# Optimization experiments

Hardware: AMD Instinct MI355X
Metric: run time of the kernel (lower is better)

Reference implementation:

```python
import jax, jax.numpy as jnp
import numpy as np
import math

NUM_HEADS = 16
MAX_BIAS = 8.0

def _alibi_slopes(n_heads):
    def slopes(n):
        start = 2.0 ** (-2 ** (-(math.log2(n) - 3)))
        return [start * start ** i for i in range(n)]
    if math.log2(n_heads).is_integer():
        s = slopes(n_heads)
    else:
        p = 2 ** math.floor(math.log2(n_heads))
        s = slopes(p) + slopes(2 * p)[0::2][: n_heads - p]
    return jnp.asarray(np.array(s, dtype=np.float32))

def setup_inputs() -> dict:
    key = jax.random.key(0)
    ks = jax.random.split(key, 5)
    B, S, C = 2, 2048, 1024
    return {
        "x": jax.random.normal(ks[0], (B, S, C), jnp.float32),
        "in_proj_weight": jax.random.normal(ks[1], (3 * C, C), jnp.float32) * (C ** -0.5),
        "in_proj_bias": jax.random.normal(ks[2], (3 * C,), jnp.float32) * 0.02,
        "out_proj_weight": jax.random.normal(ks[3], (C, C), jnp.float32) * (C ** -0.5),
        "out_proj_bias": jax.random.normal(ks[4], (C,), jnp.float32) * 0.02,
    }

def reference(x, in_proj_weight, in_proj_bias, out_proj_weight, out_proj_bias):
    B, S, C = x.shape
    H = NUM_HEADS
    D = C // H
    # fused qkv projection: [B,S,3C] -> [3,B,H,S,D]
    qkv = x @ in_proj_weight.T + in_proj_bias
    qkv = qkv.reshape(B, S, 3, H, D).transpose(2, 0, 3, 1, 4)
    q, k, v = qkv[0], qkv[1], qkv[2]
    # ALiBi bias: slopes[h] * (i - j), clamped above at MAX_BIAS -> [H,S,S]
    slopes = _alibi_slopes(H)
    pos = jnp.arange(S, dtype=jnp.float32)
    rel = pos[:, None] - pos[None, :]  # [S,S]
    bias = jnp.minimum(rel[None, :, :] * slopes[:, None, None], MAX_BIAS)
    # scores [B,H,S,S]
    scores = jnp.einsum("bhqd,bhkd->bhqk", q, k) * (D ** -0.5) + bias[None]
    probs = jax.nn.softmax(scores, axis=-1)
    out = jnp.einsum("bhqk,bhkd->bhqd", probs, v)
    out = out.transpose(0, 2, 1, 3).reshape(B, S, C)
    return out @ out_proj_weight.T + out_proj_bias
```

## Files before the change

### kernel.cpp

```cpp
#include <hip/hip_runtime.h>
#include <hip/hip_bf16.h>

typedef __bf16 bf16;
typedef __bf16 bf16x8 __attribute__((ext_vector_type(8)));
typedef __bf16 bf16x4 __attribute__((ext_vector_type(4)));
typedef float  f32x4  __attribute__((ext_vector_type(4)));

#define LOG2E 1.44269504088896340736f


__device__ __forceinline__ void gl_lds16(const void* g, void* l) {
  __builtin_amdgcn_global_load_lds((__attribute__((address_space(1))) void*)g,
                                   (__attribute__((address_space(3))) void*)l,
                                   16, 0, 0);
}

__global__ void cvt3_kernel(const float* __restrict__ x,
                            const float* __restrict__ w1,
                            const float* __restrict__ w2,
                            bf16* __restrict__ xb,
                            bf16* __restrict__ w1b,
                            bf16* __restrict__ w2b) {
  const int NX = 1048576, NW1 = 786432, NW2 = 262144;
  const int total = NX + NW1 + NW2;
  int i = blockIdx.x * blockDim.x + threadIdx.x;
  const int stride = gridDim.x * blockDim.x;
  for (; i < total; i += stride) {
    const float* s; bf16* d; int j;
    if (i < NX)            { s = x;  d = xb;  j = i; }
    else if (i < NX + NW1) { s = w1; d = w1b; j = i - NX; }
    else                   { s = w2; d = w2b; j = i - NX - NW1; }
    f32x4 v = ((const f32x4*)s)[j];
    bf16x4 o;
    o[0] = (bf16)v[0]; o[1] = (bf16)v[1]; o[2] = (bf16)v[2]; o[3] = (bf16)v[3];
    ((bf16x4*)d)[j] = o;
  }
}

template<int EPI>
__global__ __launch_bounds__(256) void gemm_bt(const bf16* __restrict__ A,
                                               const bf16* __restrict__ Bw,
                                               const float* __restrict__ bias,
                                               void* __restrict__ outp,
                                               int M, int N, int K) {
  __shared__ bf16 As[128 * 64];
  __shared__ bf16 Bs[128 * 64];
  const int tid  = threadIdx.x;
  const int lane = tid & 63;
  const int w    = tid >> 6;
  const int wm   = w >> 1, wn = w & 1;
  const int mBase = blockIdx.y * 128;
  const int nBase = blockIdx.x * 128;
  const int rl = lane & 15;
  const int qg = lane >> 4;
  const int srow = tid >> 3;
  const int schunk = tid & 7;

  f32x4 acc[4][4] = {};

  for (int k0 = 0; k0 < K; k0 += 64) {
    __syncthreads();
#pragma unroll
    for (int rr = 0; rr < 4; ++rr) {
      int r  = rr * 32 + srow;
      int cs = schunk ^ (r & 7);
      gl_lds16(A  + (size_t)(mBase + r) * K + k0 + cs * 8, As + r * 64 + schunk * 8);
      gl_lds16(Bw + (size_t)(nBase + r) * K + k0 + cs * 8, Bs + r * 64 + schunk * 8);
    }
    __syncthreads();
#pragma unroll
    for (int ks = 0; ks < 2; ++ks) {
      bf16x8 af[4], bfr[4];
      const int cl = ks * 4 + qg;
#pragma unroll
      for (int mf = 0; mf < 4; ++mf) {
        int r = wm * 64 + mf * 16 + rl;
        af[mf] = *(const bf16x8*)(As + r * 64 + (cl ^ (r & 7)) * 8);
      }
#pragma unroll
      for (int nf = 0; nf < 4; ++nf) {
        int r = wn * 64 + nf * 16 + rl;
        bfr[nf] = *(const bf16x8*)(Bs + r * 64 + (cl ^ (r & 7)) * 8);
      }
#pragma unroll
      for (int mf = 0; mf < 4; ++mf)
#pragma unroll
        for (int nf = 0; nf < 4; ++nf)
          acc[mf][nf] = __builtin_amdgcn_mfma_f32_16x16x32_bf16(af[mf], bfr[nf],
                                                                acc[mf][nf], 0, 0, 0);
    }
  }

#pragma unroll
  for (int mf = 0; mf < 4; ++mf) {
#pragma unroll
    for (int nf = 0; nf < 4; ++nf) {
      int n = nBase + wn * 64 + nf * 16 + rl;
      float bv = bias[n];
#pragma unroll
      for (int j = 0; j < 4; ++j) {
        int m = mBase + wm * 64 + mf * 16 + qg * 4 + j;
        float val = acc[mf][nf][j] + bv;
        if (EPI == 0) {
          int t = n >> 10, rem = n & 1023;
          int h = rem >> 6, d = rem & 63;
          int b = m >> 11, s = m & 2047;
          bf16* q = (bf16*)outp;
          size_t hb = (size_t)(b * 16 + h);
          if (t == 0) {
            q[(hb * 2048 + s) * 64 + d] = (bf16)(val * (0.125f * LOG2E));
          } else if (t == 1) {
            q[4194304 + (hb * 2048 + s) * 64 + d] = (bf16)val;
          } else {
            q[8388608 + (hb * 64 + d) * 2048 + s] = (bf16)val;
          }
        } else {
          ((float*)outp)[(size_t)m * N + n] = val;
        }
      }
    }
  }
}

__global__ __launch_bounds__(256) void attn_kernel(const bf16* __restrict__ qkv,
                                                   bf16* __restrict__ attout) {
  constexpr int S = 2048;
  __shared__ bf16 Ks[64 * 64];
  __shared__ bf16 Vt[80 * 64];
  __shared__ bf16 Ps[4][16 * 72];

  const int tid  = threadIdx.x;
  const int lane = tid & 63;
  const int w    = tid >> 6;
  const int qt   = blockIdx.x;
  const int bh   = blockIdx.y;
  const int h    = bh & 15;
  const size_t headoff = (size_t)bh * 131072;
  const bf16* Qg = qkv + headoff;
  const bf16* Kg = qkv + 4194304 + headoff;
  const bf16* Vg = qkv + 8388608 + headoff;

  const int rl = lane & 15;
  const int qg = lane >> 4;
  const int srow = tid >> 3;
  const int schunk = tid & 7;

  for (int i = tid; i < 16 * 64; i += 256)
    Vt[64 * 64 + i] = (i < 64) ? (bf16)1.0f : (bf16)0.0f;

  bf16x8 qf[2];
  {
    int row = qt * 64 + w * 16 + rl;
    qf[0] = *(const bf16x8*)(Qg + (size_t)row * 64 + qg * 8);
    qf[1] = *(const bf16x8*)(Qg + (size_t)row * 64 + 32 + qg * 8);
  }

  const float slope2 = exp2f(-0.5f * (float)(h + 1)) * LOG2E;
  const float MB2 = 8.0f * LOG2E;
  float arow[4], bcol[4];
#pragma unroll
  for (int j = 0; j < 4; ++j)
    arow[j] = slope2 * (float)(qt * 64 + w * 16 + qg * 4 + j);
#pragma unroll
  for (int cf = 0; cf < 4; ++cf)
    bcol[cf] = slope2 * (float)(cf * 16 + rl);
  const float kstep = slope2 * 64.0f;

  f32x4 o[5] = {};
  float m2[4];
#pragma unroll
  for (int j = 0; j < 4; ++j) m2[j] = -__builtin_inff();

  for (int kb = 0; kb < S; kb += 64) {
    __syncthreads();
#pragma unroll
    for (int rr = 0; rr < 2; ++rr) {
      int r  = rr * 32 + srow;
      int cs = schunk ^ (r & 7);
      gl_lds16(Kg + (size_t)(kb + r) * 64 + cs * 8, Ks + r * 64 + schunk * 8);
      gl_lds16(Vg + (size_t)r * 2048 + kb + cs * 8, Vt + r * 64 + schunk * 8);
    }
    __syncthreads();

    f32x4 sc[4] = {};
#pragma unroll
    for (int cf = 0; cf < 4; ++cf) {
      int r = cf * 16 + rl;
#pragma unroll
      for (int ks = 0; ks < 2; ++ks) {
        int cl = ks * 4 + qg;
        bf16x8 kf = *(const bf16x8*)(Ks + r * 64 + (cl ^ (r & 7)) * 8);
        sc[cf] = __builtin_amdgcn_mfma_f32_16x16x32_bf16(qf[ks], kf, sc[cf], 0, 0, 0);
      }
    }

    float pv[4][4], mx[4];
#pragma unroll
    for (int j = 0; j < 4; ++j) mx[j] = -__builtin_inff();
#pragma unroll
    for (int cf = 0; cf < 4; ++cf)
#pragma unroll
      for (int j = 0; j < 4; ++j) {
        float t = sc[cf][j] + fminf(arow[j] - bcol[cf], MB2);
        pv[cf][j] = t;
        mx[j] = fmaxf(mx[j], t);
      }
#pragma unroll
    for (int off = 1; off < 16; off <<= 1)
#pragma unroll
      for (int j = 0; j < 4; ++j)
        mx[j] = fmaxf(mx[j], __shfl_xor(mx[j], off, 16));

    float g = fmaxf(fmaxf(mx[0] - m2[0], mx[1] - m2[1]),
                    fmaxf(mx[2] - m2[2], mx[3] - m2[3]));
    g = fmaxf(g, __shfl_xor(g, 16));
    g = fmaxf(g, __shfl_xor(g, 32));
    if (g > 8.0f) {
#pragma unroll
      for (int j = 0; j < 4; ++j) {
        float mn = fmaxf(m2[j], mx[j]);
        float alpha = exp2f(m2[j] - mn);
        m2[j] = mn;
#pragma unroll
        for (int dg = 0; dg < 5; ++dg)
          o[dg][j] *= alpha;
      }
    }

#pragma unroll
    for (int cf = 0; cf < 4; ++cf)
#pragma unroll
      for (int j = 0; j < 4; ++j) {
        float p = exp2f(pv[cf][j] - m2[j]);
        Ps[w][(qg * 4 + j) * 72 + cf * 16 + rl] = (bf16)p;
      }

    __builtin_amdgcn_wave_barrier();

#pragma unroll
    for (int kc = 0; kc < 2; ++kc) {
      bf16x8 pa = *(const bf16x8*)(&Ps[w][rl * 72 + kc * 32 + qg * 8]);
#pragma unroll
      for (int dg = 0; dg < 5; ++dg) {
        int row = dg * 16 + rl;
        bf16x8 vb = *(const bf16x8*)(Vt + row * 64 + ((kc * 4 + qg) ^ (row & 7)) * 8);
        o[dg] = __builtin_amdgcn_mfma_f32_16x16x32_bf16(pa, vb, o[dg], 0, 0, 0);
      }
    }

#pragma unroll
    for (int cf = 0; cf < 4; ++cf) bcol[cf] += kstep;
  }

  float inv[4];
#pragma unroll
  for (int j = 0; j < 4; ++j)
    inv[j] = 1.0f / __shfl(o[4][j], lane & 48);

  const int b = bh >> 4;
#pragma unroll
  for (int dg = 0; dg < 4; ++dg)
#pragma unroll
    for (int j = 0; j < 4; ++j) {
      int row = qt * 64 + w * 16 + qg * 4 + j;
      int col = h * 64 + dg * 16 + rl;
      attout[((size_t)b * 2048 + row) * 1024 + col] = (bf16)(o[dg][j] * inv[j]);
    }
}

extern "C" void kernel_launch(void* const* d_in, const int* in_sizes, int n_in,
                              void* d_out, int out_size, void* d_ws, size_t ws_size,
                              hipStream_t stream) {
  const float* x  = (const float*)d_in[0];
  const float* w1 = (const float*)d_in[1];
  const float* b1 = (const float*)d_in[2];
  const float* w2 = (const float*)d_in[3];
  const float* b2 = (const float*)d_in[4];
  float* out = (float*)d_out;

  char* ws = (char*)d_ws;
  bf16* xb    = (bf16*)(ws);
  bf16* w1b   = (bf16*)(ws + 8388608);
  bf16* w2b   = (bf16*)(ws + 14680064);
  bf16* qkvb  = (bf16*)(ws + 16777216);
  bf16* attnb = (bf16*)(ws + 41943040);

  cvt3_kernel<<<2048, 256, 0, stream>>>(x, w1, w2, xb, w1b, w2b);
  gemm_bt<0><<<dim3(24, 32), 256, 0, stream>>>(xb, w1b, b1, (void*)qkvb, 4096, 3072, 1024);
  attn_kernel<<<dim3(32, 32), 256, 0, stream>>>(qkvb, attnb);
  gemm_bt<1><<<dim3(8, 32), 256, 0, stream>>>(attnb, w2b, b2, (void*)out, 4096, 1024, 1024);
}
```

Measured before the change: 171.0 us.

## Keep softmax probabilities in registers via transposed QK^T and 16x16x16 MFMA for PV

Swaps the QK^T MFMA operands so each lane holds scores in the layout needed as the A operand of a 16x16x16 bf16 MFMA. The probabilities then feed PV straight from registers, which removes the per-wave LDS staging buffer and its wave barrier. The online softmax is reduced to a single wave-wide max with a shared rescale, and the bias term is folded into a running base offset. The change also precomputes LDS offsets, remaps blocks so heads interleave, and fills the extra V rows with ones for the row sum. In exchange it uses twice as many smaller MFMAs for PV and a coarser shared max, which carries some numerical risk.

```diff
diff --git a/kernel.cpp b/kernel.cpp
--- a/kernel.cpp
+++ b/kernel.cpp
@@ -5,6 +5,7 @@
 typedef __bf16 bf16x8 __attribute__((ext_vector_type(8)));
 typedef __bf16 bf16x4 __attribute__((ext_vector_type(4)));
 typedef float  f32x4  __attribute__((ext_vector_type(4)));
+typedef short  s16x4  __attribute__((ext_vector_type(4)));
 
 #define LOG2E 1.44269504088896340736f
 
@@ -13,6 +14,23 @@
   __builtin_amdgcn_global_load_lds((__attribute__((address_space(1))) void*)g,
                                    (__attribute__((address_space(3))) void*)l,
                                    16, 0, 0);
+}
+
+#if __has_builtin(__builtin_amdgcn_mfma_f32_16x16x16bf16_1k)
+__device__ __forceinline__ f32x4 mfma16(s16x4 a, s16x4 b, f32x4 c) {
+  return __builtin_amdgcn_mfma_f32_16x16x16bf16_1k(a, b, c, 0, 0, 0);
+}
+#else
+__device__ __forceinline__ f32x4 mfma16(s16x4 a, s16x4 b, f32x4 c) {
+  f32x4 d;
+  asm volatile("v_mfma_f32_16x16x16_bf16 %0, %1, %2, %3\n\ts_nop 7\n\ts_nop 3"
+               : "=v"(d) : "v"(a), "v"(b), "v"(c));
+  return d;
+}
+#endif
+
+__device__ __forceinline__ s16x4 as_s16x4(bf16x4 v) {
+  union { bf16x4 h; s16x4 s; } u; u.h = v; return u.s;
 }
 
 __global__ void cvt3_kernel(const float* __restrict__ x,
@@ -127,14 +145,14 @@
   constexpr int S = 2048;
   __shared__ bf16 Ks[64 * 64];
   __shared__ bf16 Vt[80 * 64];
-  __shared__ bf16 Ps[4][16 * 72];
 
   const int tid  = threadIdx.x;
   const int lane = tid & 63;
   const int w    = tid >> 6;
-  const int qt   = blockIdx.x;
-  const int bh   = blockIdx.y;
-  const int h    = bh & 15;
+  const int id = blockIdx.x;
+  const int bh = (id & 7) * 4 + ((id >> 3) & 3);
+  const int qt = id >> 5;
+  const int h  = bh & 15;
   const size_t headoff = (size_t)bh * 131072;
   const bf16* Qg = qkv + headoff;
   const bf16* Kg = qkv + 4194304 + headoff;
@@ -146,116 +164,121 @@
   const int schunk = tid & 7;
 
   for (int i = tid; i < 16 * 64; i += 256)
-    Vt[64 * 64 + i] = (i < 64) ? (bf16)1.0f : (bf16)0.0f;
-
+    Vt[64 * 64 + i] = (bf16)1.0f;
+
+  const int qrow = qt * 64 + w * 16 + rl;
   bf16x8 qf[2];
-  {
-    int row = qt * 64 + w * 16 + rl;
-    qf[0] = *(const bf16x8*)(Qg + (size_t)row * 64 + qg * 8);
-    qf[1] = *(const bf16x8*)(Qg + (size_t)row * 64 + 32 + qg * 8);
-  }
+  qf[0] = *(const bf16x8*)(Qg + (size_t)qrow * 64 + qg * 8);
+  qf[1] = *(const bf16x8*)(Qg + (size_t)qrow * 64 + 32 + qg * 8);
+
+  int koff[4][2];
+#pragma unroll
+  for (int cf = 0; cf < 4; ++cf) {
+    int r = cf * 16 + rl, r7 = r & 7;
+#pragma unroll
+    for (int ks = 0; ks < 2; ++ks)
+      koff[cf][ks] = r * 64 + (((ks * 4 + qg) ^ r7) << 3);
+  }
+  int voff[4][5];
+#pragma unroll
+  for (int dg = 0; dg < 5; ++dg) {
+    int row = dg * 16 + rl, r7 = row & 7;
+#pragma unroll
+    for (int cf = 0; cf < 4; ++cf)
+      voff[cf][dg] = row * 64 + ((((cf << 1) + (qg >> 1)) ^ r7) << 3) + ((qg & 1) << 2);
+  }
+
+  const int cs8 = (schunk ^ (srow & 7)) * 8;
+  const bf16* ksrc = Kg + (size_t)srow * 64 + cs8;
+  const bf16* vsrc = Vg + (size_t)srow * 2048 + cs8;
+  bf16* kdst = Ks + srow * 64 + schunk * 8;
+  bf16* vdst = Vt + srow * 64 + schunk * 8;
 
   const float slope2 = exp2f(-0.5f * (float)(h + 1)) * LOG2E;
-  const float MB2 = 8.0f * LOG2E;
-  float arow[4], bcol[4];
+  const float nslope = -slope2;
+  const float kstep  = slope2 * 64.0f;
+  float basep = slope2 * (float)(qrow - qg * 4);
+  float Mm    = 8.0f * LOG2E;
+
+  f32x4 o[5] = {};
+
+  for (int kt = 0; kt < S / 64; ++kt) {
+    __syncthreads();
+    gl_lds16(ksrc,             kdst);
+    gl_lds16(ksrc + 32 * 64,   kdst + 32 * 64);
+    gl_lds16(vsrc,             vdst);
+    gl_lds16(vsrc + 32 * 2048, vdst + 32 * 64);
+    ksrc += 64 * 64; vsrc += 64;
+    __syncthreads();
+
+    f32x4 sc[4] = {};
+#pragma unroll
+    for (int cf = 0; cf < 4; ++cf)
+#pragma unroll
+      for (int ks = 0; ks < 2; ++ks) {
+        bf16x8 kf = *(const bf16x8*)(Ks + koff[cf][ks]);
+        sc[cf] = __builtin_amdgcn_mfma_f32_16x16x32_bf16(kf, qf[ks], sc[cf], 0, 0, 0);
+      }
+
+    float t[4][4];
+#pragma unroll
+    for (int cf = 0; cf < 4; ++cf)
+#pragma unroll
+      for (int j = 0; j < 4; ++j)
+        t[cf][j] = sc[cf][j] + fminf(__builtin_fmaf(nslope, (float)(cf * 16 + j), basep), Mm);
+
+    float mxa = fmaxf(fmaxf(t[0][0], t[0][1]), fmaxf(t[0][2], t[0][3]));
+    float mxb = fmaxf(fmaxf(t[1][0], t[1][1]), fmaxf(t[1][2], t[1][3]));
+    float mxc = fmaxf(fmaxf(t[2][0], t[2][1]), fmaxf(t[2][2], t[2][3]));
+    float mxd = fmaxf(fmaxf(t[3][0], t[3][1]), fmaxf(t[3][2], t[3][3]));
+    float mx = fmaxf(fmaxf(mxa, mxb), fmaxf(mxc, mxd));
+    mx = fmaxf(mx, __shfl_xor(mx, 16));
+    mx = fmaxf(mx, __shfl_xor(mx, 32));
+
+    bf16x4 pav[4];
+    if (__any(mx > 8.0f)) {
+      float d = fmaxf(mx, 0.0f);
+      basep -= d; Mm -= d;
+      float alpha = exp2f(-d);
+      float av[4];
+#pragma unroll
+      for (int j = 0; j < 4; ++j)
+        av[j] = __shfl(alpha, qg * 4 + j);
+#pragma unroll
+      for (int dg = 0; dg < 5; ++dg)
+#pragma unroll
+        for (int j = 0; j < 4; ++j)
+          o[dg][j] *= av[j];
+#pragma unroll
+      for (int cf = 0; cf < 4; ++cf)
+#pragma unroll
+        for (int j = 0; j < 4; ++j)
+          pav[cf][j] = (bf16)exp2f(t[cf][j] - d);
+    } else {
+#pragma unroll
+      for (int cf = 0; cf < 4; ++cf)
+#pragma unroll
+        for (int j = 0; j < 4; ++j)
+          pav[cf][j] = (bf16)exp2f(t[cf][j]);
+    }
+
+#pragma unroll
+    for (int cf = 0; cf < 4; ++cf) {
+      s16x4 pa = as_s16x4(pav[cf]);
+#pragma unroll
+      for (int dg = 0; dg < 5; ++dg) {
+        s16x4 vb = *(const s16x4*)(Vt + voff[cf][dg]);
+        o[dg] = mfma16(pa, vb, o[dg]);
+      }
+    }
+
+    basep -= kstep;
+  }
+
+  float inv[4];
 #pragma unroll
   for (int j = 0; j < 4; ++j)
-    arow[j] = slope2 * (float)(qt * 64 + w * 16 + qg * 4 + j);
-#pragma unroll
-  for (int cf = 0; cf < 4; ++cf)
-    bcol[cf] = slope2 * (float)(cf * 16 + rl);
-  const float kstep = slope2 * 64.0f;
-
-  f32x4 o[5] = {};
-  float m2[4];
-#pragma unroll
-  for (int j = 0; j < 4; ++j) m2[j] = -__builtin_inff();
-
-  for (int kb = 0; kb < S; kb += 64) {
-    __syncthreads();
-#pragma unroll
-    for (int rr = 0; rr < 2; ++rr) {
-      int r  = rr * 32 + srow;
-      int cs = schunk ^ (r & 7);
-      gl_lds16(Kg + (size_t)(kb + r) * 64 + cs * 8, Ks + r * 64 + schunk * 8);
-      gl_lds16(Vg + (size_t)r * 2048 + kb + cs * 8, Vt + r * 64 + schunk * 8);
-    }
-    __syncthreads();
-
-    f32x4 sc[4] = {};
-#pragma unroll
-    for (int cf = 0; cf < 4; ++cf) {
-      int r = cf * 16 + rl;
-#pragma unroll
-      for (int ks = 0; ks < 2; ++ks) {
-        int cl = ks * 4 + qg;
-        bf16x8 kf = *(const bf16x8*)(Ks + r * 64 + (cl ^ (r & 7)) * 8);
-        sc[cf] = __builtin_amdgcn_mfma_f32_16x16x32_bf16(qf[ks], kf, sc[cf], 0, 0, 0);
-      }
-    }
-
-    float pv[4][4], mx[4];
-#pragma unroll
-    for (int j = 0; j < 4; ++j) mx[j] = -__builtin_inff();
-#pragma unroll
-    for (int cf = 0; cf < 4; ++cf)
-#pragma unroll
-      for (int j = 0; j < 4; ++j) {
-        float t = sc[cf][j] + fminf(arow[j] - bcol[cf], MB2);
-        pv[cf][j] = t;
-        mx[j] = fmaxf(mx[j], t);
-      }
-#pragma unroll
-    for (int off = 1; off < 16; off <<= 1)
-#pragma unroll
-      for (int j = 0; j < 4; ++j)
-        mx[j] = fmaxf(mx[j], __shfl_xor(mx[j], off, 16));
-
-    float g = fmaxf(fmaxf(mx[0] - m2[0], mx[1] - m2[1]),
-                    fmaxf(mx[2] - m2[2], mx[3] - m2[3]));
-    g = fmaxf(g, __shfl_xor(g, 16));
-    g = fmaxf(g, __shfl_xor(g, 32));
-    if (g > 8.0f) {
-#pragma unroll
-      for (int j = 0; j < 4; ++j) {
-        float mn = fmaxf(m2[j], mx[j]);
-        float alpha = exp2f(m2[j] - mn);
-        m2[j] = mn;
-#pragma unroll
-        for (int dg = 0; dg < 5; ++dg)
-          o[dg][j] *= alpha;
-      }
-    }
-
-#pragma unroll
-    for (int cf = 0; cf < 4; ++cf)
-#pragma unroll
-      for (int j = 0; j < 4; ++j) {
-        float p = exp2f(pv[cf][j] - m2[j]);
-        Ps[w][(qg * 4 + j) * 72 + cf * 16 + rl] = (bf16)p;
-      }
-
-    __builtin_amdgcn_wave_barrier();
-
-#pragma unroll
-    for (int kc = 0; kc < 2; ++kc) {
-      bf16x8 pa = *(const bf16x8*)(&Ps[w][rl * 72 + kc * 32 + qg * 8]);
-#pragma unroll
-      for (int dg = 0; dg < 5; ++dg) {
-        int row = dg * 16 + rl;
-        bf16x8 vb = *(const bf16x8*)(Vt + row * 64 + ((kc * 4 + qg) ^ (row & 7)) * 8);
-        o[dg] = __builtin_amdgcn_mfma_f32_16x16x32_bf16(pa, vb, o[dg], 0, 0, 0);
-      }
-    }
-
-#pragma unroll
-    for (int cf = 0; cf < 4; ++cf) bcol[cf] += kstep;
-  }
-
-  float inv[4];
-#pragma unroll
-  for (int j = 0; j < 4; ++j)
-    inv[j] = 1.0f / __shfl(o[4][j], lane & 48);
+    inv[j] = 1.0f / o[4][j];
 
   const int b = bh >> 4;
 #pragma unroll
@@ -287,6 +310,6 @@
 
   cvt3_kernel<<<2048, 256, 0, stream>>>(x, w1, w2, xb, w1b, w2b);
   gemm_bt<0><<<dim3(24, 32), 256, 0, stream>>>(xb, w1b, b1, (void*)qkvb, 4096, 3072, 1024);
-  attn_kernel<<<dim3(32, 32), 256, 0, stream>>>(qkvb, attnb);
+  attn_kernel<<<1024, 256, 0, stream>>>(qkvb, attnb);
   gemm_bt<1><<<dim3(8, 32), 256, 0, stream>>>(attnb, w2b, b2, (void*)out, 4096, 1024, 1024);
 }
```

Measured after the change: 168.4 us. No clear change (-1.5%).
